# Kernel tuning notes

Hardware: AMD Instinct MI355X
Metric: run time of the kernel (lower is better)

Reference implementation:

```python
import jax, jax.numpy as jnp
import numpy as np


def _moie_block(x, w, b, alpha, activation):
    # x: [B, in], w: [K, in, out], b: [K, out], alpha: [B, K]
    z = jnp.einsum('bi,kio->bko', x, w) + b          # [B, K, out] per-expert outputs
    combined = jnp.einsum('bko,bk->bo', z, alpha)    # alpha-weighted sum over experts
    if activation:
        combined = jax.nn.relu(combined)
    return combined


def setup_inputs() -> dict:
    key = jax.random.key(0)
    ks = jax.random.split(key, 8)
    B, D, K, H = 16384, 512, 8, 512
    s = 0.02  # weight init scale
    return {
        'x': jax.random.normal(ks[0], (B, D), jnp.float32),
        'gate_w': jax.random.normal(ks[1], (D, K), jnp.float32) * s,
        'gate_b': jnp.zeros((K,), jnp.float32),
        'w0': jax.random.normal(ks[2], (K, D, H), jnp.float32) * s,
        'b0': jnp.zeros((K, H), jnp.float32),
        'w1': jax.random.normal(ks[3], (K, H, H), jnp.float32) * s,
        'b1': jnp.zeros((K, H), jnp.float32),
        'w2': jax.random.normal(ks[4], (K, H, H), jnp.float32) * s,
        'b2': jnp.zeros((K, H), jnp.float32),
        'wo': jax.random.normal(ks[5], (K, H, D), jnp.float32) * s,
        'bo': jnp.zeros((K, D), jnp.float32),
    }


def reference(x, gate_w, gate_b, w0, b0, w1, b1, w2, b2, wo, bo):
    # Gating: softmax(Linear(x)) -> alpha [B, K]; same alpha reused at every layer.
    alpha = jax.nn.softmax(x @ gate_w + gate_b, axis=-1)
    # n_blocks=3 hidden MoIE blocks: MoIEBlock (no act) -> ReLU -> Dropout(0, eval=identity)
    h = _moie_block(x, w0, b0, alpha, activation=True)
    h = _moie_block(h, w1, b1, alpha, activation=True)
    h = _moie_block(h, w2, b2, alpha, activation=True)
    # Output MoIEBlock: no activation
    return _moie_block(h, wo, bo, alpha, activation=False)
```

## Files before the change

kernel.cpp:

```cpp
#include <hip/hip_runtime.h>
#include <stdint.h>

typedef _Float16 f16;
typedef _Float16 f16x8 __attribute__((ext_vector_type(8)));
typedef float f32x4 __attribute__((ext_vector_type(4)));

#define NROWS 16384
#define DIM   512
#define NEXP  8
#define BM    128
#define BN    128
#define BK    32
#define NKS   16
#define WSTRIDE (DIM*DIM)

#define GLOAD16(gp, lp) __builtin_amdgcn_global_load_lds( \
    (const __attribute__((address_space(1))) void*)(gp),  \
    (__attribute__((address_space(3))) void*)(lp), 16, 0, 0)

#define MFMA16(a,b,c) __builtin_amdgcn_mfma_f32_16x16x32_f16(a, b, c, 0, 0, 0)

__global__ __launch_bounds__(256) void convert_w(
    const float* __restrict__ w0, const float* __restrict__ w1,
    const float* __restrict__ w2, const float* __restrict__ wo,
    f16* __restrict__ Wt)
{
    __shared__ float tile[32][33];
    int b  = blockIdx.x;
    int m  = b >> 8;
    int bi = (b >> 4) & 15;
    int bj = b & 15;
    int layer = m >> 3;
    const float* src =
        (layer == 0 ? w0 : layer == 1 ? w1 : layer == 2 ? w2 : wo)
        + (size_t)(m & 7) * DIM * DIM;
    f16* dst = Wt + (size_t)m * DIM * DIM;
    int tx = threadIdx.x & 31, ty = threadIdx.x >> 5;
#pragma unroll
    for (int r = 0; r < 4; ++r)
        tile[ty + 8*r][tx] = src[(size_t)(bi*32 + ty + 8*r) * DIM + bj*32 + tx];
    __syncthreads();
#pragma unroll
    for (int r = 0; r < 4; ++r)
        dst[(size_t)(bj*32 + ty + 8*r) * DIM + bi*32 + tx] = (f16)tile[tx][ty + 8*r];
}

__global__ __launch_bounds__(256) void gate_kernel(
    const float* __restrict__ x, const float* __restrict__ gw,
    const float* __restrict__ gb, float* __restrict__ alpha,
    f16* __restrict__ xh)
{
    int tid = threadIdx.x, lane = tid & 63, wid = tid >> 6;
    int row = blockIdx.x * 4 + wid;
    const float* xr = x + (size_t)row * DIM;
    float acc[8] = {0,0,0,0,0,0,0,0};
    float xv[8];
#pragma unroll
    for (int j = 0; j < 8; ++j) {
        int d = lane + 64*j;
        float v = xr[d];
        xv[j] = v;
        const float4* g = (const float4*)(gw + (size_t)d * 8);
        float4 g0 = g[0], g1 = g[1];
        acc[0] += v*g0.x; acc[1] += v*g0.y; acc[2] += v*g0.z; acc[3] += v*g0.w;
        acc[4] += v*g1.x; acc[5] += v*g1.y; acc[6] += v*g1.z; acc[7] += v*g1.w;
    }
#pragma unroll
    for (int mlane = 32; mlane >= 1; mlane >>= 1) {
#pragma unroll
        for (int k = 0; k < 8; ++k) acc[k] += __shfl_xor(acc[k], mlane, 64);
    }
#pragma unroll
    for (int k = 0; k < 8; ++k) acc[k] += gb[k];
    float mx = acc[0];
#pragma unroll
    for (int k = 1; k < 8; ++k) mx = fmaxf(mx, acc[k]);
    float s = 0.f;
#pragma unroll
    for (int k = 0; k < 8; ++k) { acc[k] = __expf(acc[k] - mx); s += acc[k]; }
    float inv = 1.0f / s;
    if (lane == 0) {
        float4 a0 = {acc[0]*inv, acc[1]*inv, acc[2]*inv, acc[3]*inv};
        float4 a1 = {acc[4]*inv, acc[5]*inv, acc[6]*inv, acc[7]*inv};
        *(float4*)(alpha + (size_t)row*8)     = a0;
        *(float4*)(alpha + (size_t)row*8 + 4) = a1;
    }
#pragma unroll
    for (int j = 0; j < 8; ++j)
        xh[(size_t)row * DIM + lane + 64*j] = (f16)xv[j];
}


#define ESTEP(WAITN, ISSUE, SLOT, EIDX) \
    asm volatile("s_waitcnt vmcnt(" #WAITN ")" ::: "memory"); \
    __builtin_amdgcn_s_barrier(); \
    ISSUE \
    { const f16* Bb = Ball + (SLOT)*4096 + bOff; \
      f16x8 bf0 = *(const f16x8*)(Bb); \
      f16x8 bf1 = *(const f16x8*)(Bb + 512); \
      f16x8 bf2 = *(const f16x8*)(Bb + 1024); \
      f16x8 bf3 = *(const f16x8*)(Bb + 1536); \
      f16 s0_ = salh0[EIDX], s1_ = salh1[EIDX], s2_ = salh2[EIDX], s3_ = salh3[EIDX]; \
      f16x8 a0 = af0 * (f16x8){s0_,s0_,s0_,s0_,s0_,s0_,s0_,s0_}; \
      f16x8 a1 = af1 * (f16x8){s1_,s1_,s1_,s1_,s1_,s1_,s1_,s1_}; \
      f16x8 a2 = af2 * (f16x8){s2_,s2_,s2_,s2_,s2_,s2_,s2_,s2_}; \
      f16x8 a3 = af3 * (f16x8){s3_,s3_,s3_,s3_,s3_,s3_,s3_,s3_}; \
      __builtin_amdgcn_s_setprio(1); \
      acc[0][0]=MFMA16(a0,bf0,acc[0][0]); acc[0][1]=MFMA16(a0,bf1,acc[0][1]); \
      acc[0][2]=MFMA16(a0,bf2,acc[0][2]); acc[0][3]=MFMA16(a0,bf3,acc[0][3]); \
      acc[1][0]=MFMA16(a1,bf0,acc[1][0]); acc[1][1]=MFMA16(a1,bf1,acc[1][1]); \
      acc[1][2]=MFMA16(a1,bf2,acc[1][2]); acc[1][3]=MFMA16(a1,bf3,acc[1][3]); \
      acc[2][0]=MFMA16(a2,bf0,acc[2][0]); acc[2][1]=MFMA16(a2,bf1,acc[2][1]); \
      acc[2][2]=MFMA16(a2,bf2,acc[2][2]); acc[2][3]=MFMA16(a2,bf3,acc[2][3]); \
      acc[3][0]=MFMA16(a3,bf0,acc[3][0]); acc[3][1]=MFMA16(a3,bf1,acc[3][1]); \
      acc[3][2]=MFMA16(a3,bf2,acc[3][2]); acc[3][3]=MFMA16(a3,bf3,acc[3][3]); \
      __builtin_amdgcn_s_setprio(0); }

#define READ_AF(P) \
      af0 = *(const f16x8*)((P) + aOff); \
      af1 = *(const f16x8*)((P) + aOff + 512); \
      af2 = *(const f16x8*)((P) + aOff + 1024); \
      af3 = *(const f16x8*)((P) + aOff + 1536);

#define STG_B(KS, EXP, SLOT) \
      GLOAD16(bSrc + (size_t)(EXP)*WSTRIDE + (KS)*BK,          bD + (SLOT)*4096); \
      GLOAD16(bSrc + (size_t)(EXP)*WSTRIDE + (KS)*BK + 64*DIM, bD + (SLOT)*4096 + 2048);
#define STG_A(KS, DST) \
      GLOAD16(aSrc + (KS)*BK,          DST); \
      GLOAD16(aSrc + (KS)*BK + 64*DIM, DST + 2048);

template<int RELU, int OUTF32>
__global__ __launch_bounds__(256, 2) void moie_gemm(
    const f16*  __restrict__ A,
    const f16*  __restrict__ Wt,
    const float* __restrict__ alpha,
    const float* __restrict__ bias,
    f16*  __restrict__ Hout,
    float* __restrict__ Fout)
{
    __shared__ __align__(16) f16 Abuf[2][BM*BK];
    __shared__ __align__(16) f16 Bbuf[4][BN*BK];
    __shared__ float alpha_s[BM*9];
    __shared__ float bias_s[NEXP*BN];

    int bid = blockIdx.x;
    int swz = (bid & 7) * 64 + (bid >> 3);
    int cb = swz >> 7, rb = swz & 127;
    int rowBase = rb * BM, colBase = cb * BN;
    int tid = threadIdx.x, lane = tid & 63, wid = tid >> 6;
    int wm = wid >> 1, wn = wid & 1;

    for (int i = tid; i < BM*NEXP; i += 256)
        alpha_s[(i >> 3)*9 + (i & 7)] = alpha[(size_t)(rowBase + (i >> 3))*8 + (i & 7)];
    for (int i = tid; i < NEXP*BN; i += 256)
        bias_s[i] = bias[(i >> 7)*DIM + colBase + (i & 127)];

    int srow = tid >> 2;
    int sg   = ((tid & 3) ^ ((srow >> 1) & 3)) * 8;
    const f16* aSrc = A  + (size_t)(rowBase + srow) * DIM + sg;
    const f16* bSrc = Wt + (size_t)(colBase + srow) * DIM + sg;
    f16* aW0 = Abuf[0] + tid*8;
    f16* aW1 = Abuf[1] + tid*8;
    f16* bD  = Bbuf[0] + tid*8;
    const f16* Ball = Bbuf[0];

    int kg   = ((lane >> 4) ^ (((lane & 15) >> 1) & 3)) * 8;
    int aOff = (wm*64 + (lane & 15)) * BK + kg;
    int bOff = (wn*64 + (lane & 15)) * BK + kg;

    __syncthreads();

    STG_A(0, aW0);
    STG_B(0, 0, 0); STG_B(0, 1, 1); STG_B(0, 2, 2);

    f16 salh0[NEXP], salh1[NEXP], salh2[NEXP], salh3[NEXP];
    {
        int r0 = wm*64 + (lane & 15);
#pragma unroll
        for (int e = 0; e < NEXP; ++e) {
            salh0[e] = (f16)alpha_s[(r0     )*9 + e];
            salh1[e] = (f16)alpha_s[(r0 + 16)*9 + e];
            salh2[e] = (f16)alpha_s[(r0 + 32)*9 + e];
            salh3[e] = (f16)alpha_s[(r0 + 48)*9 + e];
        }
    }

    f16x8 af0, af1, af2, af3;
    f32x4 acc[4][4];
#pragma unroll
    for (int i = 0; i < 4; ++i)
#pragma unroll
        for (int j = 0; j < 4; ++j) acc[i][j] = (f32x4){0.f,0.f,0.f,0.f};

    for (int ss = 0; ss < NKS - 1; ++ss) {
        const f16* Ard = (ss & 1) ? Abuf[1] : Abuf[0];
        f16* an = (ss & 1) ? aW0 : aW1;
        ESTEP(4, { READ_AF(Ard); STG_B(ss, 3, 3); STG_A(ss + 1, an); }, 0, 0)
        ESTEP(6, { STG_B(ss, 4, 0); }, 1, 1)
        ESTEP(6, { STG_B(ss, 5, 1); }, 2, 2)
        ESTEP(6, { STG_B(ss, 6, 2); }, 3, 3)
        ESTEP(4, { STG_B(ss, 7, 3); }, 0, 4)
        ESTEP(4, { STG_B(ss + 1, 0, 0); }, 1, 5)
        ESTEP(4, { STG_B(ss + 1, 1, 1); }, 2, 6)
        ESTEP(4, { STG_B(ss + 1, 2, 2); }, 3, 7)
    }
    {
        ESTEP(4, { READ_AF(Abuf[1]); STG_B(15, 3, 3); }, 0, 0)
        ESTEP(4, { STG_B(15, 4, 0); }, 1, 1)
        ESTEP(4, { STG_B(15, 5, 1); }, 2, 2)
        ESTEP(4, { STG_B(15, 6, 2); }, 3, 3)
        ESTEP(4, { STG_B(15, 7, 3); }, 0, 4)
        ESTEP(4, { }, 1, 5)
        ESTEP(2, { }, 2, 6)
        ESTEP(0, { }, 3, 7)
    }

#pragma unroll
    for (int i = 0; i < 4; ++i)
#pragma unroll
        for (int q = 0; q < 4; ++q) {
            int rloc = wm*64 + i*16 + (lane >> 4)*4 + q;
            size_t row = (size_t)(rowBase + rloc);
#pragma unroll
            for (int j = 0; j < 4; ++j) {
                int cloc = wn*64 + j*16 + (lane & 15);
                float v = acc[i][j][q];
#pragma unroll
                for (int e2 = 0; e2 < NEXP; ++e2)
                    v += alpha_s[rloc*9 + e2] * bias_s[e2*BN + cloc];
                if (RELU) v = fmaxf(v, 0.f);
                if (OUTF32) Fout[row*DIM + colBase + cloc] = v;
                else        Hout[row*DIM + colBase + cloc] = (f16)v;
            }
        }
}

extern "C" void kernel_launch(void* const* d_in, const int* in_sizes, int n_in,
                              void* d_out, int out_size, void* d_ws, size_t ws_size,
                              hipStream_t stream)
{
    const float* x  = (const float*)d_in[0];
    const float* gw = (const float*)d_in[1];
    const float* gb = (const float*)d_in[2];
    const float* w0 = (const float*)d_in[3];
    const float* b0 = (const float*)d_in[4];
    const float* w1 = (const float*)d_in[5];
    const float* b1 = (const float*)d_in[6];
    const float* w2 = (const float*)d_in[7];
    const float* b2 = (const float*)d_in[8];
    const float* wo = (const float*)d_in[9];
    const float* bo = (const float*)d_in[10];
    float* out = (float*)d_out;

    char* ws = (char*)d_ws;
    const size_t wtBytes = (size_t)4 * NEXP * DIM * DIM * sizeof(f16);
    f16*   Wt    = (f16*)ws;
    float* alpha = (float*)(ws + wtBytes);
    f16*   h0    = (f16*)(ws + wtBytes + (size_t)NROWS*NEXP*sizeof(float));
    f16*   h1    = h0 + (size_t)NROWS * DIM;
    const size_t L = (size_t)NEXP * DIM * DIM;

    convert_w<<<8192, 256, 0, stream>>>(w0, w1, w2, wo, Wt);
    gate_kernel<<<NROWS/4, 256, 0, stream>>>(x, gw, gb, alpha, h0);

    moie_gemm<1,0><<<512, 256, 0, stream>>>(h0, Wt,       alpha, b0, h1, nullptr);
    moie_gemm<1,0><<<512, 256, 0, stream>>>(h1, Wt + L,   alpha, b1, h0, nullptr);
    moie_gemm<1,0><<<512, 256, 0, stream>>>(h0, Wt + 2*L, alpha, b2, h1, nullptr);
    moie_gemm<0,1><<<512, 256, 0, stream>>>(h1, Wt + 3*L, alpha, bo, nullptr, out);
}
```

Measured before the change: 315.7 us.

## Software-pipeline LDS B-fragment reads one expert step ahead of MFMAs

Restructures the per-expert step so each phase reads the next slot's B fragments from LDS into a ping-pong register set (bfE/bfO) before issuing MFMAs on the previously loaded set. The global-to-LDS issue moves after the MFMAs, and the prologue now stages four B slots. The goal is to hide LDS read latency behind matrix math, at the cost of extra VGPRs and a more delicate vmcnt/barrier schedule that must still guard against slot reuse hazards.

```diff
diff --git a/kernel.cpp b/kernel.cpp
--- a/kernel.cpp
+++ b/kernel.cpp
@@ -91,36 +91,36 @@
 }
 
 
-#define ESTEP(WAITN, ISSUE, SLOT, EIDX) \
-    asm volatile("s_waitcnt vmcnt(" #WAITN ")" ::: "memory"); \
-    __builtin_amdgcn_s_barrier(); \
-    ISSUE \
-    { const f16* Bb = Ball + (SLOT)*4096 + bOff; \
-      f16x8 bf0 = *(const f16x8*)(Bb); \
-      f16x8 bf1 = *(const f16x8*)(Bb + 512); \
-      f16x8 bf2 = *(const f16x8*)(Bb + 1024); \
-      f16x8 bf3 = *(const f16x8*)(Bb + 1536); \
-      f16 s0_ = salh0[EIDX], s1_ = salh1[EIDX], s2_ = salh2[EIDX], s3_ = salh3[EIDX]; \
-      f16x8 a0 = af0 * (f16x8){s0_,s0_,s0_,s0_,s0_,s0_,s0_,s0_}; \
-      f16x8 a1 = af1 * (f16x8){s1_,s1_,s1_,s1_,s1_,s1_,s1_,s1_}; \
-      f16x8 a2 = af2 * (f16x8){s2_,s2_,s2_,s2_,s2_,s2_,s2_,s2_}; \
-      f16x8 a3 = af3 * (f16x8){s3_,s3_,s3_,s3_,s3_,s3_,s3_,s3_}; \
-      __builtin_amdgcn_s_setprio(1); \
-      acc[0][0]=MFMA16(a0,bf0,acc[0][0]); acc[0][1]=MFMA16(a0,bf1,acc[0][1]); \
-      acc[0][2]=MFMA16(a0,bf2,acc[0][2]); acc[0][3]=MFMA16(a0,bf3,acc[0][3]); \
-      acc[1][0]=MFMA16(a1,bf0,acc[1][0]); acc[1][1]=MFMA16(a1,bf1,acc[1][1]); \
-      acc[1][2]=MFMA16(a1,bf2,acc[1][2]); acc[1][3]=MFMA16(a1,bf3,acc[1][3]); \
-      acc[2][0]=MFMA16(a2,bf0,acc[2][0]); acc[2][1]=MFMA16(a2,bf1,acc[2][1]); \
-      acc[2][2]=MFMA16(a2,bf2,acc[2][2]); acc[2][3]=MFMA16(a2,bf3,acc[2][3]); \
-      acc[3][0]=MFMA16(a3,bf0,acc[3][0]); acc[3][1]=MFMA16(a3,bf1,acc[3][1]); \
-      acc[3][2]=MFMA16(a3,bf2,acc[3][2]); acc[3][3]=MFMA16(a3,bf3,acc[3][3]); \
-      __builtin_amdgcn_s_setprio(0); }
+#define READ_BF(B, SLOT) \
+      B##0 = *(const f16x8*)(Ball + (SLOT)*4096 + bOff); \
+      B##1 = *(const f16x8*)(Ball + (SLOT)*4096 + bOff + 512); \
+      B##2 = *(const f16x8*)(Ball + (SLOT)*4096 + bOff + 1024); \
+      B##3 = *(const f16x8*)(Ball + (SLOT)*4096 + bOff + 1536);
 
 #define READ_AF(P) \
       af0 = *(const f16x8*)((P) + aOff); \
       af1 = *(const f16x8*)((P) + aOff + 512); \
       af2 = *(const f16x8*)((P) + aOff + 1024); \
       af3 = *(const f16x8*)((P) + aOff + 1536);
+
+#define MULS(E) { \
+      f16 s0_ = salh0[E], s1_ = salh1[E], s2_ = salh2[E], s3_ = salh3[E]; \
+      a0 = af0 * (f16x8){s0_,s0_,s0_,s0_,s0_,s0_,s0_,s0_}; \
+      a1 = af1 * (f16x8){s1_,s1_,s1_,s1_,s1_,s1_,s1_,s1_}; \
+      a2 = af2 * (f16x8){s2_,s2_,s2_,s2_,s2_,s2_,s2_,s2_}; \
+      a3 = af3 * (f16x8){s3_,s3_,s3_,s3_,s3_,s3_,s3_,s3_}; }
+
+#define MFMA16x(B) \
+      __builtin_amdgcn_s_setprio(1); \
+      acc[0][0]=MFMA16(a0,B##0,acc[0][0]); acc[0][1]=MFMA16(a0,B##1,acc[0][1]); \
+      acc[0][2]=MFMA16(a0,B##2,acc[0][2]); acc[0][3]=MFMA16(a0,B##3,acc[0][3]); \
+      acc[1][0]=MFMA16(a1,B##0,acc[1][0]); acc[1][1]=MFMA16(a1,B##1,acc[1][1]); \
+      acc[1][2]=MFMA16(a1,B##2,acc[1][2]); acc[1][3]=MFMA16(a1,B##3,acc[1][3]); \
+      acc[2][0]=MFMA16(a2,B##0,acc[2][0]); acc[2][1]=MFMA16(a2,B##1,acc[2][1]); \
+      acc[2][2]=MFMA16(a2,B##2,acc[2][2]); acc[2][3]=MFMA16(a2,B##3,acc[2][3]); \
+      acc[3][0]=MFMA16(a3,B##0,acc[3][0]); acc[3][1]=MFMA16(a3,B##1,acc[3][1]); \
+      acc[3][2]=MFMA16(a3,B##2,acc[3][2]); acc[3][3]=MFMA16(a3,B##3,acc[3][3]); \
+      __builtin_amdgcn_s_setprio(0);
 
 #define STG_B(KS, EXP, SLOT) \
       GLOAD16(bSrc + (size_t)(EXP)*WSTRIDE + (KS)*BK,          bD + (SLOT)*4096); \
@@ -128,6 +128,14 @@
 #define STG_A(KS, DST) \
       GLOAD16(aSrc + (KS)*BK,          DST); \
       GLOAD16(aSrc + (KS)*BK + 64*DIM, DST + 2048);
+
+#define PH(WAITN, BR, RSLOT, BMM, EIDX, ISSUE) \
+    asm volatile("s_waitcnt vmcnt(" #WAITN ")" ::: "memory"); \
+    __builtin_amdgcn_s_barrier(); \
+    READ_BF(BR, RSLOT) \
+    MULS(EIDX) \
+    MFMA16x(BMM) \
+    ISSUE
 
 template<int RELU, int OUTF32>
 __global__ __launch_bounds__(256, 2) void moie_gemm(
@@ -171,7 +179,7 @@
     __syncthreads();
 
     STG_A(0, aW0);
-    STG_B(0, 0, 0); STG_B(0, 1, 1); STG_B(0, 2, 2);
+    STG_B(0, 0, 0); STG_B(0, 1, 1); STG_B(0, 2, 2); STG_B(0, 3, 3);
 
     f16 salh0[NEXP], salh1[NEXP], salh2[NEXP], salh3[NEXP];
     {
@@ -185,34 +193,47 @@
         }
     }
 
-    f16x8 af0, af1, af2, af3;
+    f16x8 af0, af1, af2, af3, a0, a1, a2, a3;
+    f16x8 bfE0, bfE1, bfE2, bfE3, bfO0, bfO1, bfO2, bfO3;
     f32x4 acc[4][4];
 #pragma unroll
     for (int i = 0; i < 4; ++i)
 #pragma unroll
         for (int j = 0; j < 4; ++j) acc[i][j] = (f32x4){0.f,0.f,0.f,0.f};
 
+    asm volatile("s_waitcnt vmcnt(6)" ::: "memory");
+    __builtin_amdgcn_s_barrier();
+    READ_AF(Abuf[0]);
+    READ_BF(bfE, 0);
+
     for (int ss = 0; ss < NKS - 1; ++ss) {
-        const f16* Ard = (ss & 1) ? Abuf[1] : Abuf[0];
         f16* an = (ss & 1) ? aW0 : aW1;
-        ESTEP(4, { READ_AF(Ard); STG_B(ss, 3, 3); STG_A(ss + 1, an); }, 0, 0)
-        ESTEP(6, { STG_B(ss, 4, 0); }, 1, 1)
-        ESTEP(6, { STG_B(ss, 5, 1); }, 2, 2)
-        ESTEP(6, { STG_B(ss, 6, 2); }, 3, 3)
-        ESTEP(4, { STG_B(ss, 7, 3); }, 0, 4)
-        ESTEP(4, { STG_B(ss + 1, 0, 0); }, 1, 5)
-        ESTEP(4, { STG_B(ss + 1, 1, 1); }, 2, 6)
-        ESTEP(4, { STG_B(ss + 1, 2, 2); }, 3, 7)
+        const f16* Anx = (ss & 1) ? Abuf[0] : Abuf[1];
+        PH(4, bfO, 1, bfE, 0, { STG_B(ss, 4, 0); })
+        PH(4, bfE, 2, bfO, 1, { STG_B(ss, 5, 1); })
+        PH(4, bfO, 3, bfE, 2, { STG_B(ss, 6, 2); })
+        PH(4, bfE, 0, bfO, 3, { STG_B(ss, 7, 3); STG_A(ss + 1, an); })
+        PH(6, bfO, 1, bfE, 4, { STG_B(ss + 1, 0, 0); })
+        PH(6, bfE, 2, bfO, 5, { STG_B(ss + 1, 1, 1); })
+        PH(6, bfO, 3, bfE, 6, { STG_B(ss + 1, 2, 2); })
+        asm volatile("s_waitcnt vmcnt(4)" ::: "memory");
+        __builtin_amdgcn_s_barrier();
+        READ_BF(bfE, 0)
+        MULS(7)
+        MFMA16x(bfO)
+        READ_AF(Anx);
+        STG_B(ss + 1, 3, 3);
     }
     {
-        ESTEP(4, { READ_AF(Abuf[1]); STG_B(15, 3, 3); }, 0, 0)
-        ESTEP(4, { STG_B(15, 4, 0); }, 1, 1)
-        ESTEP(4, { STG_B(15, 5, 1); }, 2, 2)
-        ESTEP(4, { STG_B(15, 6, 2); }, 3, 3)
-        ESTEP(4, { STG_B(15, 7, 3); }, 0, 4)
-        ESTEP(4, { }, 1, 5)
-        ESTEP(2, { }, 2, 6)
-        ESTEP(0, { }, 3, 7)
+        PH(4, bfO, 1, bfE, 0, { STG_B(15, 4, 0); })
+        PH(4, bfE, 2, bfO, 1, { STG_B(15, 5, 1); })
+        PH(4, bfO, 3, bfE, 2, { STG_B(15, 6, 2); })
+        PH(4, bfE, 0, bfO, 3, { STG_B(15, 7, 3); })
+        PH(4, bfO, 1, bfE, 4, { })
+        PH(2, bfE, 2, bfO, 5, { })
+        PH(0, bfO, 3, bfE, 6, { })
+        MULS(7)
+        MFMA16x(bfO)
     }
 
 #pragma unroll
```

New measurement: 682.5 us. 2.16x slower.
